# Optimization experiments

Measured on AMD Instinct MI355X. Metric: run time of the kernel, lower is better.

## Reference

```python
import jax, jax.numpy as jnp
import numpy as np

N_ENTITIES = 100000
EMBED = 64
BATCH = 4096
TEMPERATURE = 0.2


def _infonce(v1, v2, temperature):
    # v1, v2: [B, d]
    B = v1.shape[0]
    sim11 = v1 @ v1.T  # [B,B]
    sim22 = v2 @ v2.T
    sim12 = v1 @ v2.T
    eye = jnp.eye(B, dtype=bool)
    neg_inf = jnp.float32(-jnp.inf)
    sim11 = jnp.where(eye, neg_inf, sim11)
    sim22 = jnp.where(eye, neg_inf, sim22)
    logits1 = jnp.concatenate([sim12, sim11], axis=-1)          # [B,2B]
    logits2 = jnp.concatenate([sim22, sim12.T], axis=-1)        # [B,2B]
    logits = jnp.concatenate([logits1, logits2], axis=0) / temperature  # [2B,2B]
    targets = jnp.arange(2 * B)
    logp = jax.nn.log_softmax(logits, axis=-1)
    return -jnp.mean(jnp.take_along_axis(logp, targets[:, None], axis=-1))


def setup_inputs() -> dict:
    key = jax.random.key(0)
    k1, k2, k3, k4, k5, k6 = jax.random.split(key, 6)
    return {
        "input_u_list": jax.random.randint(k1, (BATCH,), 0, N_ENTITIES),
        "input_i_list": jax.random.randint(k2, (BATCH,), 0, N_ENTITIES),
        "u_sub1_embeddings": jax.random.normal(k3, (N_ENTITIES, EMBED), dtype=jnp.float32),
        "i_sub1_embeddings": jax.random.normal(k4, (N_ENTITIES, EMBED), dtype=jnp.float32),
        "u_sub2_embeddings": jax.random.normal(k5, (N_ENTITIES, EMBED), dtype=jnp.float32),
        "i_sub2_embeddings": jax.random.normal(k6, (N_ENTITIES, EMBED), dtype=jnp.float32),
    }


def reference(input_u_list, input_i_list, u_sub1_embeddings, i_sub1_embeddings,
              u_sub2_embeddings, i_sub2_embeddings):
    # user branch: gather + L2-normalize
    u1 = u_sub1_embeddings[input_u_list]
    u2 = u_sub2_embeddings[input_u_list]
    u1 = u1 / jnp.linalg.norm(u1, axis=1, keepdims=True)
    u2 = u2 / jnp.linalg.norm(u2, axis=1, keepdims=True)
    user_cl_loss = _infonce(u1, u2, TEMPERATURE)
    # item branch: gather only (the original does NOT normalize items)
    i1 = i_sub1_embeddings[input_i_list]
    i2 = i_sub2_embeddings[input_i_list]
    item_cl_loss = _infonce(i1, i2, TEMPERATURE)
    return user_cl_loss + item_cl_loss
```

## Files before the change

### kernel.cpp

```cpp
#include <hip/hip_runtime.h>
#include <hip/hip_bf16.h>
#include <math.h>

#define B_SZ   4096
#define D      64
#define RPB    8192
#define NCHUNK 8
#define TPC    8
#define NPART  16
#define LN2    0.69314718055994531f
#define PRESCALE 2.6857914f
#define DEFER_THR 60.0f

typedef __attribute__((ext_vector_type(8))) short  bf16x8;
typedef __attribute__((ext_vector_type(4))) float  f32x4;

__device__ __forceinline__ float fexp2(float x) { return __builtin_amdgcn_exp2f(x); }

typedef const __attribute__((address_space(1))) unsigned int* gptr_t;
typedef __attribute__((address_space(3))) unsigned int* lptr_t;
__device__ __forceinline__ void stage16(const void* g, void* l) {
    __builtin_amdgcn_global_load_lds((gptr_t)g, (lptr_t)l, 16, 0, 0);
}


__global__ __launch_bounds__(256) void gather_kernel(
    const int* __restrict__ u_idx, const int* __restrict__ i_idx,
    const float* __restrict__ u1e, const float* __restrict__ i1e,
    const float* __restrict__ u2e, const float* __restrict__ i2e,
    __hip_bfloat16* __restrict__ Xbf, float* __restrict__ dots,
    float* __restrict__ out)
{
    const int tid  = threadIdx.x;
    if (blockIdx.x == 0 && tid == 0) *out = 0.f;
    const int wave = tid >> 6, lane = tid & 63;
    const int g      = blockIdx.x * 4 + wave;
    const int branch = g >> 12;
    const int i      = g & (B_SZ - 1);
    const int idx    = (branch == 0) ? u_idx[i] : i_idx[i];
    const float* s1  = (branch == 0) ? u1e : i1e;
    const float* s2  = (branch == 0) ? u2e : i2e;

    float v1 = s1[(size_t)idx * D + lane];
    float v2 = s2[(size_t)idx * D + lane];
    if (branch == 0) {
        float a = v1 * v1, b = v2 * v2;
        #pragma unroll
        for (int o = 32; o > 0; o >>= 1) {
            a += __shfl_xor(a, o, 64);
            b += __shfl_xor(b, o, 64);
        }
        v1 *= rsqrtf(a);
        v2 *= rsqrtf(b);
    }
    float p = v1 * v2;
    #pragma unroll
    for (int o = 32; o > 0; o >>= 1) p += __shfl_xor(p, o, 64);
    if (lane == 0) dots[g] = p;

    const size_t row1 = (size_t)branch * RPB + i;
    Xbf[row1 * D + lane]          = __float2bfloat16(v1 * PRESCALE);
    Xbf[(row1 + B_SZ) * D + lane] = __float2bfloat16(v2 * PRESCALE);
}

template<int IS_USER>
__device__ __forceinline__ void gram_body(
    const __hip_bfloat16* __restrict__ Xb, float2* __restrict__ P,
    const int bx, const int cp, char* sm)
{
    const int tid  = threadIdx.x;
    const int r0   = bx * 128;
    const int wave = tid >> 6, lane = tid & 63;
    const int wm = wave >> 1, wn = wave & 1;
    const int quad = lane >> 4, tx = lane & 15;

    const int srow_b = wave * 32 + (lane >> 3);
    const int scb    = ((lane & 7) * 16) ^ ((lane >> 3) << 4);
    const char* Xbytes = (const char*)Xb;

    {
        const char* src = Xbytes + (size_t)(cp * TPC) * 16384;
        #pragma unroll
        for (int k = 0; k < 4; ++k)
            stage16(src + (srow_b + k * 8) * 128 + scb,
                    sm + wave * 4096 + k * 1024);
    }

    bf16x8 afr[4][2];
    const __hip_bfloat16* Ap = Xb + (size_t)(r0 + wm * 64 + tx) * D + quad * 8;
    #pragma unroll
    for (int mt = 0; mt < 4; ++mt)
        #pragma unroll
        for (int ks = 0; ks < 2; ++ks)
            afr[mt][ks] = *(const bf16x8*)(Ap + mt * 16 * D + ks * 32);

    float m_run[16], s_run[16];
    #pragma unroll
    for (int r = 0; r < 16; ++r) { m_run[r] = -INFINITY; s_run[r] = 0.f; }

    const int lrq  = wm * 64 + quad * 4;
    const int lcol = wn * 64 + tx;

    const int rbase = (wn * 64 + tx) * 128;
    const int key   = (tx & 7) << 4;
    const int cb0   = (quad * 16) ^ key;
    const int cb1   = (64 + quad * 16) ^ key;

    __syncthreads();

    #pragma unroll 1
    for (int g = 0; g < 16; ++g) {
        const int t     = g & 7;
        const int chunk = cp + (g >> 3) * 4;
        const int ct    = chunk * TPC + t;
        const int cur   = (g & 1) << 14;

        if (g + 1 < 16) {
            const int gn  = g + 1;
            const int ctn = (cp + (gn >> 3) * 4) * TPC + (gn & 7);
            const char* src = Xbytes + (size_t)ctn * 16384;
            char* dst = sm + ((gn & 1) << 14) + wave * 4096;
            #pragma unroll
            for (int k = 0; k < 4; ++k)
                stage16(src + (srow_b + k * 8) * 128 + scb, dst + k * 1024);
        }

        bf16x8 b0[4], b1[4];
        #pragma unroll
        for (int nt = 0; nt < 4; ++nt) {
            b0[nt] = *(const bf16x8*)(sm + cur + rbase + nt * 2048 + cb0);
            b1[nt] = *(const bf16x8*)(sm + cur + rbase + nt * 2048 + cb1);
        }

        f32x4 acc[4][4];
        const f32x4 z = {0.f, 0.f, 0.f, 0.f};
        #pragma unroll
        for (int nt = 0; nt < 4; ++nt)
            #pragma unroll
            for (int mt = 0; mt < 4; ++mt)
                acc[mt][nt] = __builtin_amdgcn_mfma_f32_16x16x32_bf16(afr[mt][0], b0[nt], z, 0, 0, 0);
        #pragma unroll
        for (int nt = 0; nt < 4; ++nt)
            #pragma unroll
            for (int mt = 0; mt < 4; ++mt)
                acc[mt][nt] = __builtin_amdgcn_mfma_f32_16x16x32_bf16(afr[mt][1], b1[nt], acc[mt][nt], 0, 0, 0);

        const bool diag = (ct == bx);
        #pragma unroll
        for (int mt = 0; mt < 4; ++mt) {
            #pragma unroll
            for (int rr = 0; rr < 4; ++rr) {
                float y0 = acc[mt][0][rr], y1 = acc[mt][1][rr],
                      y2 = acc[mt][2][rr], y3 = acc[mt][3][rr];
                if (diag) {
                    const int dr = lrq + mt * 16 + rr - lcol;
                    if (dr == 0)  y0 = -INFINITY;
                    if (dr == 16) y1 = -INFINITY;
                    if (dr == 32) y2 = -INFINITY;
                    if (dr == 48) y3 = -INFINITY;
                }
                const int r = mt * 4 + rr;
                if (IS_USER) {
                    s_run[r] += fexp2(y0) + fexp2(y1) + fexp2(y2) + fexp2(y3);
                } else {
                    float mx = fmaxf(fmaxf(y0, y1), fmaxf(y2, y3));
                    if (__builtin_expect(mx > m_run[r] + DEFER_THR, 0)) {
                        s_run[r] *= fexp2(m_run[r] - mx);
                        m_run[r] = mx;
                    }
                    const float m = m_run[r];
                    s_run[r] += fexp2(y0 - m) + fexp2(y1 - m)
                              + fexp2(y2 - m) + fexp2(y3 - m);
                }
            }
        }

        if (t == 7) {
            #pragma unroll
            for (int r = 0; r < 16; ++r) {
                float m = IS_USER ? 0.f : m_run[r];
                float s = s_run[r];
                #pragma unroll
                for (int o = 1; o < 16; o <<= 1) {
                    if (IS_USER) {
                        s += __shfl_xor(s, o, 64);
                    } else {
                        float om = __shfl_xor(m, o, 64);
                        float os = __shfl_xor(s, o, 64);
                        float M  = fmaxf(m, om);
                        s = s * fexp2(m - M) + os * fexp2(om - M);
                        m = M;
                    }
                }
                if (tx == 0) {
                    const int grow = r0 + wm * 64 + (r >> 2) * 16 + quad * 4 + (r & 3);
                    P[(size_t)grow * NPART + chunk * 2 + wn] = make_float2(m, s);
                }
                m_run[r] = -INFINITY;
                s_run[r] = 0.f;
            }
        }

        __syncthreads();
    }
}

__global__ __launch_bounds__(256, 3) void gram_lse_fused(
    const __hip_bfloat16* __restrict__ Xb0, float2* __restrict__ P0)
{
    __shared__ __align__(16) char sm[32768];
    const int bid    = blockIdx.x;
    const int branch = bid & 1;
    const int bx     = (bid >> 1) & 63;
    const int cp     = bid >> 7;
    const __hip_bfloat16* Xb = Xb0 + (size_t)branch * RPB * D;
    float2* P = P0 + (size_t)branch * RPB * NPART;
    if (branch == 0) gram_body<1>(Xb, P, bx, cp, sm);
    else             gram_body<0>(Xb, P, bx, cp, sm);
}

__global__ __launch_bounds__(256) void merge_kernel(
    const float2* __restrict__ P, const float* __restrict__ dots,
    float* __restrict__ out)
{
    __shared__ float red[4];
    const int tid  = threadIdx.x;
    const int wave = tid >> 6, lane = tid & 63;

    float vsum = 0.f;
    #pragma unroll
    for (int k = 0; k < 8; ++k) {
        const int vb  = blockIdx.x * 8 + k;
        const int gw  = vb * 4 + wave;
        const int row = gw * 4 + (lane >> 4);
        const int c   = lane & 15;

        float2 p = P[(size_t)row * NPART + c];
        float m = p.x, s = p.y;
        #pragma unroll
        for (int o = 1; o < 16; o <<= 1) {
            float om = __shfl_xor(m, o, 64);
            float os = __shfl_xor(s, o, 64);
            float M  = fmaxf(m, om);
            s = s * fexp2(m - M) + os * fexp2(om - M);
            m = M;
        }

        if ((lane & 15) == 0)
            vsum += LN2 * (m + log2f(s)) * (1.0f / (float)RPB);
        if (tid < 8)
            vsum -= dots[vb * 8 + tid] * (5.0f / (float)B_SZ);
    }

    float v = vsum;
    #pragma unroll
    for (int o = 32; o > 0; o >>= 1) v += __shfl_xor(v, o, 64);
    if (lane == 0) red[wave] = v;
    __syncthreads();
    if (tid == 0)
        atomicAdd(out, red[0] + red[1] + red[2] + red[3]);
}

extern "C" void kernel_launch(void* const* d_in, const int* in_sizes, int n_in,
                              void* d_out, int out_size, void* d_ws, size_t ws_size,
                              hipStream_t stream) {
    const int*   u_idx = (const int*)d_in[0];
    const int*   i_idx = (const int*)d_in[1];
    const float* u1e   = (const float*)d_in[2];
    const float* i1e   = (const float*)d_in[3];
    const float* u2e   = (const float*)d_in[4];
    const float* i2e   = (const float*)d_in[5];
    float* out = (float*)d_out;

    __hip_bfloat16* Xbf = (__hip_bfloat16*)d_ws;
    float*  dots = (float*)((char*)d_ws + 2 * RPB * D * 2);
    float2* P    = (float2*)((char*)dots + RPB * sizeof(float));

    gather_kernel<<<dim3(2048), dim3(256), 0, stream>>>(
        u_idx, i_idx, u1e, i1e, u2e, i2e, Xbf, dots, out);
    gram_lse_fused<<<dim3(512), dim3(256), 0, stream>>>(Xbf, P);
    merge_kernel<<<dim3(128), dim3(256), 0, stream>>>(P, dots, out);
}
```

Baseline: 179.6 us.

## Split column tiles into six uneven chunks per block for better occupancy

Each block of the fused gram/LSE kernel now handles one contiguous run of 10 or 11 column tiles, instead of two chunks of 8 tiles. The grid grows from 512 to 768 blocks, and each block writes its partial (max, sum) once at the end. The merge kernel masks the unused partial slots 12-15 with zeros. The aim is to fill the 256 CUs more evenly and drop the mid-loop flush, at the cost of uneven per-block work and reliance on the zero (m=0, s=0) padding combining correctly in the log-sum-exp merge.

```diff
diff --git a/kernel.cpp b/kernel.cpp
--- a/kernel.cpp
+++ b/kernel.cpp
@@ -5,8 +5,7 @@
 #define B_SZ   4096
 #define D      64
 #define RPB    8192
-#define NCHUNK 8
-#define TPC    8
+#define NCHUNK 6
 #define NPART  16
 #define LN2    0.69314718055994531f
 #define PRESCALE 2.6857914f
@@ -66,7 +65,7 @@
 template<int IS_USER>
 __device__ __forceinline__ void gram_body(
     const __hip_bfloat16* __restrict__ Xb, float2* __restrict__ P,
-    const int bx, const int cp, char* sm)
+    const int bx, const int chunk, char* sm)
 {
     const int tid  = threadIdx.x;
     const int r0   = bx * 128;
@@ -74,12 +73,15 @@
     const int wm = wave >> 1, wn = wave & 1;
     const int quad = lane >> 4, tx = lane & 15;
 
+    const int cstart = chunk * 11 - (chunk > 4 ? chunk - 4 : 0);
+    const int ntile  = (chunk < 4) ? 11 : 10;
+
     const int srow_b = wave * 32 + (lane >> 3);
     const int scb    = ((lane & 7) * 16) ^ ((lane >> 3) << 4);
     const char* Xbytes = (const char*)Xb;
 
     {
-        const char* src = Xbytes + (size_t)(cp * TPC) * 16384;
+        const char* src = Xbytes + (size_t)cstart * 16384;
         #pragma unroll
         for (int k = 0; k < 4; ++k)
             stage16(src + (srow_b + k * 8) * 128 + scb,
@@ -109,17 +111,13 @@
     __syncthreads();
 
     #pragma unroll 1
-    for (int g = 0; g < 16; ++g) {
-        const int t     = g & 7;
-        const int chunk = cp + (g >> 3) * 4;
-        const int ct    = chunk * TPC + t;
-        const int cur   = (g & 1) << 14;
-
-        if (g + 1 < 16) {
-            const int gn  = g + 1;
-            const int ctn = (cp + (gn >> 3) * 4) * TPC + (gn & 7);
-            const char* src = Xbytes + (size_t)ctn * 16384;
-            char* dst = sm + ((gn & 1) << 14) + wave * 4096;
+    for (int t = 0; t < ntile; ++t) {
+        const int ct  = cstart + t;
+        const int cur = (t & 1) << 14;
+
+        if (t + 1 < ntile) {
+            const char* src = Xbytes + (size_t)(ct + 1) * 16384;
+            char* dst = sm + (((t + 1) & 1) << 14) + wave * 4096;
             #pragma unroll
             for (int k = 0; k < 4; ++k)
                 stage16(src + (srow_b + k * 8) * 128 + scb, dst + k * 1024);
@@ -175,33 +173,29 @@
             }
         }
 
-        if (t == 7) {
-            #pragma unroll
-            for (int r = 0; r < 16; ++r) {
-                float m = IS_USER ? 0.f : m_run[r];
-                float s = s_run[r];
-                #pragma unroll
-                for (int o = 1; o < 16; o <<= 1) {
-                    if (IS_USER) {
-                        s += __shfl_xor(s, o, 64);
-                    } else {
-                        float om = __shfl_xor(m, o, 64);
-                        float os = __shfl_xor(s, o, 64);
-                        float M  = fmaxf(m, om);
-                        s = s * fexp2(m - M) + os * fexp2(om - M);
-                        m = M;
-                    }
-                }
-                if (tx == 0) {
-                    const int grow = r0 + wm * 64 + (r >> 2) * 16 + quad * 4 + (r & 3);
-                    P[(size_t)grow * NPART + chunk * 2 + wn] = make_float2(m, s);
-                }
-                m_run[r] = -INFINITY;
-                s_run[r] = 0.f;
+        __syncthreads();
+    }
+
+    #pragma unroll
+    for (int r = 0; r < 16; ++r) {
+        float m = IS_USER ? 0.f : m_run[r];
+        float s = s_run[r];
+        #pragma unroll
+        for (int o = 1; o < 16; o <<= 1) {
+            if (IS_USER) {
+                s += __shfl_xor(s, o, 64);
+            } else {
+                float om = __shfl_xor(m, o, 64);
+                float os = __shfl_xor(s, o, 64);
+                float M  = fmaxf(m, om);
+                s = s * fexp2(m - M) + os * fexp2(om - M);
+                m = M;
             }
         }
-
-        __syncthreads();
+        if (tx == 0) {
+            const int grow = r0 + wm * 64 + (r >> 2) * 16 + quad * 4 + (r & 3);
+            P[(size_t)grow * NPART + chunk * 2 + wn] = make_float2(m, s);
+        }
     }
 }
 
@@ -211,12 +205,13 @@
     __shared__ __align__(16) char sm[32768];
     const int bid    = blockIdx.x;
     const int branch = bid & 1;
-    const int bx     = (bid >> 1) & 63;
-    const int cp     = bid >> 7;
+    const int rest   = bid >> 1;
+    const int bx     = rest & 63;
+    const int chunk  = rest >> 6;
     const __hip_bfloat16* Xb = Xb0 + (size_t)branch * RPB * D;
     float2* P = P0 + (size_t)branch * RPB * NPART;
-    if (branch == 0) gram_body<1>(Xb, P, bx, cp, sm);
-    else             gram_body<0>(Xb, P, bx, cp, sm);
+    if (branch == 0) gram_body<1>(Xb, P, bx, chunk, sm);
+    else             gram_body<0>(Xb, P, bx, chunk, sm);
 }
 
 __global__ __launch_bounds__(256) void merge_kernel(
@@ -235,7 +230,7 @@
         const int row = gw * 4 + (lane >> 4);
         const int c   = lane & 15;
 
-        float2 p = P[(size_t)row * NPART + c];
+        float2 p = (c < 12) ? P[(size_t)row * NPART + c] : make_float2(0.f, 0.f);
         float m = p.x, s = p.y;
         #pragma unroll
         for (int o = 1; o < 16; o <<= 1) {
@@ -278,6 +273,6 @@
 
     gather_kernel<<<dim3(2048), dim3(256), 0, stream>>>(
         u_idx, i_idx, u1e, i1e, u2e, i2e, Xbf, dots, out);
-    gram_lse_fused<<<dim3(512), dim3(256), 0, stream>>>(Xbf, P);
+    gram_lse_fused<<<dim3(768), dim3(256), 0, stream>>>(Xbf, P);
     merge_kernel<<<dim3(128), dim3(256), 0, stream>>>(P, dots, out);
 }
```

New measurement: 171.5 us. 1.05x faster.
